# Optimization experiments

Hardware: AMD Instinct MI355X
Metric: run time of the kernel (lower is better)

The kernel has to match this reference:

```python
import jax, jax.numpy as jnp
import numpy as np

B, S, HIDDEN, NH = 2, 2048, 1024, 16
D = HIDDEN // NH  # 64
PHYS_W, CONS_W = 0.2, 0.15
LN_EPS = 1e-5


def _layernorm(x, gamma, beta):
    mu = jnp.mean(x, axis=-1, keepdims=True)
    var = jnp.mean(jnp.square(x - mu), axis=-1, keepdims=True)
    return (x - mu) * jax.lax.rsqrt(var + LN_EPS) * gamma + beta


def setup_inputs() -> dict:
    key = jax.random.key(0)
    ks = jax.random.split(key, 12)
    s = 0.02
    return {
        "cnn_features": jax.random.normal(ks[0], (B, S, HIDDEN), jnp.float32),
        "llm_features": jax.random.normal(ks[1], (B, S, HIDDEN), jnp.float32),
        # Linear weights stored [in, out] so y = x @ W + b (torch's W.T)
        "Wq": jax.random.normal(ks[2], (HIDDEN, HIDDEN), jnp.float32) * s,
        "bq": jnp.zeros((HIDDEN,), jnp.float32),
        "Wk": jax.random.normal(ks[3], (HIDDEN, HIDDEN), jnp.float32) * s,
        "bk": jnp.zeros((HIDDEN,), jnp.float32),
        "Wv": jax.random.normal(ks[4], (HIDDEN, HIDDEN), jnp.float32) * s,
        "bv": jnp.zeros((HIDDEN,), jnp.float32),
        "Wo": jax.random.normal(ks[5], (HIDDEN, HIDDEN), jnp.float32) * s,
        "bo": jnp.zeros((HIDDEN,), jnp.float32),
        "energy_emb": jax.random.normal(ks[6], (1, 1, HIDDEN), jnp.float32),
        "mass_emb": jax.random.normal(ks[7], (1, 1, HIDDEN), jnp.float32),
        "momentum_emb": jax.random.normal(ks[8], (1, 1, HIDDEN), jnp.float32),
        "gamma": jnp.ones((HIDDEN,), jnp.float32),
        "beta": jnp.zeros((HIDDEN,), jnp.float32),
    }


def reference(cnn_features, llm_features, Wq, bq, Wk, bk, Wv, bv, Wo, bo,
              energy_emb, mass_emb, momentum_emb, gamma, beta):
    Bsz, Sc, _ = cnn_features.shape
    Sl = llm_features.shape[1]

    def attn(q_in, kv_in):
        Sq, Sk = q_in.shape[1], kv_in.shape[1]
        Q = (q_in @ Wq + bq).reshape(Bsz, Sq, NH, D).transpose(0, 2, 1, 3)   # bhqd
        K = (kv_in @ Wk + bk).reshape(Bsz, Sk, NH, D).transpose(0, 2, 1, 3)  # bhkd
        V = (kv_in @ Wv + bv).reshape(Bsz, Sk, NH, D).transpose(0, 2, 1, 3)  # bhkd
        scores = jnp.einsum('bhqd,bhkd->bhqk', Q, K) / np.float32(np.sqrt(D))
        # physics biases: require Sq == Sk (elementwise Q*K), shape [B,H,Sq,1]
        energy_bias = jnp.sum(Q * K, axis=-1, keepdims=True) * PHYS_W
        mass_bias = jnp.mean(Q + K, axis=-1, keepdims=True) * CONS_W
        attn_w = jax.nn.softmax(scores + energy_bias + mass_bias, axis=-1)
        attended = jnp.einsum('bhqk,bhkd->bhqd', attn_w, V)
        attended = attended.transpose(0, 2, 1, 3).reshape(Bsz, Sq, HIDDEN)
        out = attended @ Wo + bo
        return _layernorm(q_in + out, gamma, beta)

    phys = jnp.concatenate([
        jnp.broadcast_to(energy_emb, (Bsz, 1, HIDDEN)),
        jnp.broadcast_to(mass_emb, (Bsz, 1, HIDDEN)),
        jnp.broadcast_to(momentum_emb, (Bsz, 1, HIDDEN)),
    ], axis=1)  # [B, 3, HIDDEN]
    aug_cnn = jnp.concatenate([cnn_features, phys], axis=1)  # [B, Sc+3, H]
    aug_llm = jnp.concatenate([llm_features, phys], axis=1)  # [B, Sl+3, H]

    cnn_att = attn(aug_cnn, aug_llm)
    llm_att = attn(aug_llm, aug_cnn)
    return cnn_att[:, :Sc, :], llm_att[:, :Sl, :]
```

## Files before the change

### kernel.cpp

```cpp
#include <hip/hip_runtime.h>

#define BN 2
#define SS 2048
#define SA 2051
#define HID 1024
#define NHD 16
#define DH 64
#define VTLD 8320
#define KSTR 72
#define VSTR 40
#define MFMA16 __builtin_amdgcn_mfma_f32_16x16x32_bf16
#define QSCALE 0.18033688011112042f

typedef __attribute__((ext_vector_type(4))) float floatx4;
typedef __attribute__((ext_vector_type(8))) short bf16x8;
typedef __attribute__((ext_vector_type(2))) unsigned uintx2;

__device__ __forceinline__ float bf2f(short s) {
  union { unsigned u; float f; } v; v.u = ((unsigned)(unsigned short)s) << 16; return v.f;
}
__device__ __forceinline__ short f2bf(float f) {
  union { float f; unsigned u; } v; v.f = f;
  unsigned u = v.u;
  u += 0x7FFF + ((u >> 16) & 1);
  return (short)(u >> 16);
}
__device__ __forceinline__ unsigned pack2(float lo, float hi) {
  unsigned ul = __float_as_uint(lo) + 0x8000u;
  unsigned uh = __float_as_uint(hi) + 0x8000u;
  return __builtin_amdgcn_perm(uh, ul, 0x07060302u);
}
__device__ __forceinline__ unsigned cvtpk(float lo, float hi) {
  unsigned r;
  asm("v_cvt_pk_bf16_f32 %0, %1, %2" : "=v"(r) : "v"(lo), "v"(hi));
  return r;
}
__device__ __forceinline__ float exp2fast(float x) {
#if __has_builtin(__builtin_amdgcn_exp2f)
  return __builtin_amdgcn_exp2f(x);
#else
  float r; asm("v_exp_f32 %0, %1" : "=v"(r) : "v"(x)); return r;
#endif
}
__device__ __forceinline__ uintx2 qtrans(unsigned A, unsigned B) {
  auto t = __builtin_amdgcn_permlane32_swap(A, B, false, false);
  auto u = __builtin_amdgcn_permlane16_swap(t[0], t[1], false, false);
  uintx2 r; r[0] = u[0]; r[1] = u[1];
  return r;
}
__device__ __forceinline__ void gload16(const short* g, short* l) {
  __builtin_amdgcn_global_load_lds(
      (const __attribute__((address_space(1))) void*)g,
      (__attribute__((address_space(3))) void*)l, 16, 0, 0);
}
__device__ __forceinline__ bool in_is_f32(const unsigned* graw) {
  return graw[0] == 0x3F800000u;
}

__global__ __launch_bounds__(256) void convert_in2(
    const void* __restrict__ s0, const void* __restrict__ s1,
    short* __restrict__ dst, const unsigned* __restrict__ graw) {
  if (!in_is_f32(graw)) return;
  const int NF = 4096 * HID;
  int i = (blockIdx.x * 256 + threadIdx.x) * 4;
  const void* s = i < NF ? s0 : s1;
  int j = i < NF ? i : i - NF;
  float4 v = *(const float4*)((const float*)s + j);
  short4 o; o.x = f2bf(v.x); o.y = f2bf(v.y); o.z = f2bf(v.z); o.w = f2bf(v.w);
  *(short4*)(dst + i) = o;
}

__global__ __launch_bounds__(256) void convert_small(
    const void* s0, const void* s1, const void* s2, const void* s3,
    const void* s4, const void* s5, const void* s6, const void* s7,
    const void* s8, short* __restrict__ dst, const unsigned* __restrict__ graw) {
  bool f32 = in_is_f32(graw);
  const void* srcs[9] = {s0, s1, s2, s3, s4, s5, s6, s7, s8};
  const void* s = srcs[blockIdx.x];
  short* d = dst + (size_t)blockIdx.x * 1024;
  for (int i = threadIdx.x; i < 1024; i += 256)
    d[i] = f32 ? f2bf(((const float*)s)[i]) : ((const short*)s)[i];
}

__global__ __launch_bounds__(256) void conv_wt4(
    const void* __restrict__ W0, const void* __restrict__ W1,
    const void* __restrict__ W2, const void* __restrict__ W3,
    short* __restrict__ WT, const unsigned* __restrict__ graw) {
  __shared__ short tile[32][33];
  bool f32 = in_is_f32(graw);
  const void* Ws[4] = {W0, W1, W2, W3};
  const void* W = Ws[blockIdx.z];
  short* dst = WT + (size_t)blockIdx.z * HID * HID;
  int n0 = blockIdx.x * 32, k0 = blockIdx.y * 32;
  int tx = threadIdx.x & 31, ty = threadIdx.x >> 5;
#pragma unroll
  for (int i = 0; i < 4; i++) {
    int k = k0 + ty + i*8;
    short v = f32 ? f2bf(((const float*)W)[(size_t)k * HID + n0 + tx])
                  : ((const short*)W)[(size_t)k * HID + n0 + tx];
    tile[ty + i*8][tx] = v;
  }
  __syncthreads();
#pragma unroll
  for (int i = 0; i < 4; i++)
    dst[(size_t)(n0 + ty + i*8) * HID + k0 + tx] = tile[tx][ty + i*8];
}

__device__ __forceinline__ void gemm_core_3buf(
    const short* apr0, const short* apr1,
    const short* bpr0, const short* bpr1,
    short* sA, short* sB, int wave, int l16, int quad, int msub, int nsub,
    floatx4 acc[4][4]) {
  gload16(apr0, sA + wave*512);              gload16(apr1, sA + 2048 + wave*512);
  gload16(bpr0, sB + wave*512);              gload16(bpr1, sB + 2048 + wave*512);
  gload16(apr0 + 32, sA + 4096 + wave*512);  gload16(apr1 + 32, sA + 4096 + 2048 + wave*512);
  gload16(bpr0 + 32, sB + 4096 + wave*512);  gload16(bpr1 + 32, sB + 4096 + 2048 + wave*512);
  int p8 = ((quad + (l16 >> 1)) & 3) * 8;
  int cur = 0;
  for (int k0 = 0; k0 < HID; k0 += 32) {
    if (k0 + 32 < HID) {
      asm volatile("s_waitcnt vmcnt(4)" ::: "memory");
    } else {
      asm volatile("s_waitcnt vmcnt(0)" ::: "memory");
    }
    __builtin_amdgcn_s_barrier();
    __builtin_amdgcn_sched_barrier(0);
    if (k0 + 64 < HID) {
      int nx = cur == 0 ? 2 : cur - 1;
      gload16(apr0 + k0 + 64, sA + nx*4096 + wave*512);
      gload16(apr1 + k0 + 64, sA + nx*4096 + 2048 + wave*512);
      gload16(bpr0 + k0 + 64, sB + nx*4096 + wave*512);
      gload16(bpr1 + k0 + 64, sB + nx*4096 + 2048 + wave*512);
    }
    const short* cA = sA + cur*4096;
    const short* cB = sB + cur*4096;
    bf16x8 af[4], bf_[4];
#pragma unroll
    for (int i = 0; i < 4; i++) {
      af[i]  = *(const bf16x8*)(cA + (msub + i*16 + l16)*32 + p8);
      bf_[i] = *(const bf16x8*)(cB + (nsub + i*16 + l16)*32 + p8);
    }
#pragma unroll
    for (int mi = 0; mi < 4; mi++)
#pragma unroll
      for (int ni = 0; ni < 4; ni++)
        acc[mi][ni] = MFMA16(af[mi], bf_[ni], acc[mi][ni], 0, 0, 0);
    __builtin_amdgcn_sched_barrier(0);
    cur = cur == 2 ? 0 : cur + 1;
  }
}

__global__ __launch_bounds__(256) void gemm_qkv(
    const short* __restrict__ Xa, const short* __restrict__ WqT,
    const short* __restrict__ WkT, const short* __restrict__ WvT,
    const short* __restrict__ embB, const short* __restrict__ bqB,
    const short* __restrict__ bkB, const short* __restrict__ bvB,
    short* __restrict__ Qa, short* __restrict__ Ka, short* __restrict__ VT,
    const void* __restrict__ cnn, const void* __restrict__ llm,
    const unsigned* __restrict__ graw) {
  __shared__ __align__(16) short sA[3*4096];
  __shared__ __align__(16) short sB[3*4096];
  int t = threadIdx.x;
  int wave = t >> 6, lane = t & 63, l16 = lane & 15, quad = lane >> 4;
  int bid = blockIdx.x;
  int swz = (bid & 7) * 194 + (bid >> 3);
  bool f32 = in_is_f32(graw);

  const short *A, *B, *bias; short* out; long ldc;
  int m0, n0, xA, xB, tailA, tailB, bias_row; float scale;
  if (swz < 512) {
    A = nullptr; B = WqT; bias = bqB; out = Qa; ldc = HID;
    m0 = (swz >> 3) * 128; n0 = (swz & 7) * 128;
    xA = 1; xB = 0; tailA = 0; tailB = 0; bias_row = 0; scale = QSCALE;
  } else if (swz < 1032) {
    int id = swz - 512;
    A = nullptr; B = WkT; bias = bkB; out = Ka; ldc = HID;
    m0 = (id >> 3) * 128; n0 = (id & 7) * 128;
    xA = 1; xB = 0; tailA = 1; tailB = 0; bias_row = 0; scale = 1.f;
  } else {
    int id = swz - 1032;
    A = WvT; B = nullptr; bias = bvB; out = VT; ldc = VTLD;
    m0 = (id / 65) * 128; n0 = (id % 65) * 128;
    xA = 0; xB = 1; tailA = 0; tailB = 1; bias_row = 1; scale = 1.f;
  }
  int msub = (wave >> 1) * 64, nsub = (wave & 1) * 64;

  auto xrow = [&](int r) -> const short* {
    if (f32) return Xa + (size_t)r * HID;
    return r < 4096 ? (const short*)cnn + (size_t)r * HID
                    : (const short*)llm + (size_t)(r - 4096) * HID;
  };
  int kc = (((lane & 3) - ((lane >> 3) & 3)) & 3) * 8;
  const short* apr[2]; const short* bpr[2];
#pragma unroll
  for (int rep = 0; rep < 2; rep++) {
    int cid = rep * 256 + t;
    int row = cid >> 2;
    int ra = m0 + row;
    const short* ap;
    if (xA) ap = (tailA && ra >= 8192)
                   ? embB + (size_t)((ra > 8194 ? 8194 : ra) - 8192) * 1024
                   : xrow(ra);
    else    ap = A + (size_t)ra * HID;
    int rb = n0 + row;
    const short* bp;
    if (xB) bp = (tailB && rb >= 8192)
                   ? embB + (size_t)((rb > 8194 ? 8194 : rb) - 8192) * 1024
                   : xrow(rb);
    else    bp = B + (size_t)rb * HID;
    apr[rep] = ap + kc; bpr[rep] = bp + kc;
  }

  floatx4 acc[4][4] = {};
  gemm_core_3buf(apr[0], apr[1], bpr[0], bpr[1], sA, sB,
                 wave, l16, quad, msub, nsub, acc);

#pragma unroll
  for (int mi = 0; mi < 4; mi++)
#pragma unroll
    for (int ni = 0; ni < 4; ni++) {
      int col = n0 + nsub + ni*16 + l16;
      float bcol = bias_row ? 0.f : bf2f(bias[col]);
#pragma unroll
      for (int r = 0; r < 4; r++) {
        int m = m0 + msub + mi*16 + quad*4 + r;
        float v = (acc[mi][ni][r] + (bias_row ? bf2f(bias[m]) : bcol)) * scale;
        out[(size_t)m * ldc + col] = f2bf(v);
      }
    }
}

__global__ __launch_bounds__(256) void gemm_bf(
    const short* __restrict__ A, const short* __restrict__ B,
    const short* __restrict__ bias, float scale,
    float* __restrict__ out32,
    const void* __restrict__ rc0, const void* __restrict__ rc1,
    const unsigned* __restrict__ graw) {
  __shared__ __align__(16) short sA[3*4096];
  __shared__ __align__(16) short sB[3*4096];
  int t = threadIdx.x;
  int wave = t >> 6, lane = t & 63, l16 = lane & 15, quad = lane >> 4;
  int nwg = gridDim.x * gridDim.y;
  int bid = blockIdx.y * gridDim.x + blockIdx.x;
  int cpx = nwg >> 3;
  int swz = (bid & 7) * cpx + (bid >> 3);
  int bx = swz % gridDim.x, by = swz / gridDim.x;
  int m0 = by * 128, n0 = bx * 128;
  int msub = (wave >> 1) * 64, nsub = (wave & 1) * 64;

  int kc = (((lane & 3) - ((lane >> 3) & 3)) & 3) * 8;
  const short* apr[2]; const short* bpr[2];
#pragma unroll
  for (int rep = 0; rep < 2; rep++) {
    int cid = rep * 256 + t;
    int row = cid >> 2;
    apr[rep] = A + (size_t)(m0 + row) * HID + kc;
    bpr[rep] = B + (size_t)(n0 + row) * HID + kc;
  }

  floatx4 acc[4][4] = {};
  gemm_core_3buf(apr[0], apr[1], bpr[0], bpr[1], sA, sB,
                 wave, l16, quad, msub, nsub, acc);

  bool f32in = in_is_f32(graw);
#pragma unroll
  for (int mi = 0; mi < 4; mi++)
#pragma unroll
    for (int ni = 0; ni < 4; ni++) {
      int col = n0 + nsub + ni*16 + l16;
      float bcol = bf2f(bias[col]);
#pragma unroll
      for (int r = 0; r < 4; r++) {
        int m = m0 + msub + mi*16 + quad*4 + r;
        float v = (acc[mi][ni][r] + bcol) * scale;
        float res;
        if (f32in) res = ((const float*)(m < 4096 ? rc0 : rc1))[(size_t)(m & 4095) * HID + col];
        else       res = bf2f(((const short*)(m < 4096 ? rc0 : rc1))[(size_t)(m & 4095) * HID + col]);
        out32[(size_t)m * HID + col] = v + res;
      }
    }
}

__global__ __launch_bounds__(256, 2) void flash3(
    const short* __restrict__ Qa, const short* __restrict__ Ka,
    const short* __restrict__ VTa, short* __restrict__ att) {
  __shared__ __align__(16) short sK[2][2][32*KSTR];
  __shared__ __align__(16) short sV[2][2][64*VSTR];
  int t = threadIdx.x, wave = t >> 6, lane = t & 63;
  int l16 = lane & 15, quad = lane >> 4;
  int bid = blockIdx.x;
  int swz = (bid & 7) * 64 + (bid >> 3);
  int qt  = swz & 7;
  int h   = (swz >> 3) & 15;
  int sb  = swz >> 7;
  int side = sb >> 1, b = sb & 1;
  int qrow0 = side * 4096 + b * 2048;
  int kvb = (side ^ 1) * 4096 + b * 2048;
  int q0 = qt * 256 + wave * 64;

  bf16x8 qa[4], qb[4];
#pragma unroll
  for (int g = 0; g < 4; g++) {
    const short* qp = Qa + (size_t)(qrow0 + q0 + g*16 + l16) * HID + h*DH + quad*8;
    qa[g] = *(const bf16x8*)qp;
    qb[g] = *(const bf16x8*)(qp + 32);
  }

  float rs[4] = {0.f, 0.f, 0.f, 0.f};
  floatx4 o[4][4] = {};

  int krow = t >> 3, kc8 = (t & 7) * 8;
  int vrow = t >> 2, vc8 = (t & 3) * 8;
  const short* kgp = Ka + (size_t)(kvb + krow) * HID + h*DH + kc8;
  const short* vgp = VTa + (size_t)(h*DH + vrow) * VTLD + kvb + vc8;
  bf16x8 krA = *(const bf16x8*)kgp, krB = *(const bf16x8*)(kgp + 32*HID);
  bf16x8 vrA = *(const bf16x8*)vgp, vrB = *(const bf16x8*)(vgp + 32);
  int ph = 0;

  for (int kv0 = 0; kv0 < 2048; kv0 += 64) {
    *(bf16x8*)(&sK[ph][0][krow*KSTR + kc8]) = krA;
    *(bf16x8*)(&sK[ph][1][krow*KSTR + kc8]) = krB;
    *(bf16x8*)(&sV[ph][0][vrow*VSTR + vc8]) = vrA;
    *(bf16x8*)(&sV[ph][1][vrow*VSTR + vc8]) = vrB;
    __syncthreads();
    kgp += 64*HID; vgp += 64;
    krA = *(const bf16x8*)kgp; krB = *(const bf16x8*)(kgp + 32*HID);
    vrA = *(const bf16x8*)vgp; vrB = *(const bf16x8*)(vgp + 32);

#pragma unroll
    for (int s = 0; s < 2; s++) {
      const short* kw = sK[ph][s];
      const short* vw = sV[ph][s];
      bf16x8 k00 = *(const bf16x8*)(kw + l16*KSTR + quad*8);
      bf16x8 k01 = *(const bf16x8*)(kw + l16*KSTR + 32 + quad*8);
      bf16x8 k10 = *(const bf16x8*)(kw + (16 + l16)*KSTR + quad*8);
      bf16x8 k11 = *(const bf16x8*)(kw + (16 + l16)*KSTR + 32 + quad*8);
      bf16x8 v0 = *(const bf16x8*)(vw + l16*VSTR + quad*8);
      bf16x8 v1 = *(const bf16x8*)(vw + (16 + l16)*VSTR + quad*8);
      bf16x8 v2 = *(const bf16x8*)(vw + (32 + l16)*VSTR + quad*8);
      bf16x8 v3 = *(const bf16x8*)(vw + (48 + l16)*VSTR + quad*8);

#pragma unroll
      for (int g = 0; g < 4; g++) {
        floatx4 s0 = {}, s1 = {};
        __builtin_amdgcn_s_setprio(1);
        s0 = MFMA16(k00, qa[g], s0, 0, 0, 0); s0 = MFMA16(k01, qb[g], s0, 0, 0, 0);
        s1 = MFMA16(k10, qa[g], s1, 0, 0, 0); s1 = MFMA16(k11, qb[g], s1, 0, 0, 0);
        __builtin_amdgcn_s_setprio(0);

        floatx4 p0, p1;
#pragma unroll
        for (int r = 0; r < 4; r++) {
          p0[r] = exp2fast(s0[r]); p1[r] = exp2fast(s1[r]);
        }
        rs[g] += ((p0[0]+p0[1])+(p0[2]+p0[3])) + ((p1[0]+p1[1])+(p1[2]+p1[3]));

        unsigned c0 = cvtpk(p0[0], p0[1]), c1 = cvtpk(p0[2], p0[3]);
        unsigned c2 = cvtpk(p1[0], p1[1]), c3 = cvtpk(p1[2], p1[3]);
        uintx2 u0 = qtrans(c0, c2);
        uintx2 u1 = qtrans(c1, c3);
        union { unsigned u[4]; bf16x8 v; } pf;
        pf.u[0] = u0[0]; pf.u[1] = u1[0]; pf.u[2] = u0[1]; pf.u[3] = u1[1];

        __builtin_amdgcn_s_setprio(1);
        o[g][0] = MFMA16(v0, pf.v, o[g][0], 0, 0, 0);
        o[g][1] = MFMA16(v1, pf.v, o[g][1], 0, 0, 0);
        o[g][2] = MFMA16(v2, pf.v, o[g][2], 0, 0, 0);
        o[g][3] = MFMA16(v3, pf.v, o[g][3], 0, 0, 0);
        __builtin_amdgcn_s_setprio(0);
      }
    }
    ph ^= 1;
  }

  {
    int er = l16 < 2 ? l16 : 2;
    const short* kpt = Ka + (size_t)(8192 + er) * HID + h*DH + quad*8;
    bf16x8 tk0 = *(const bf16x8*)kpt;
    bf16x8 tk1 = *(const bf16x8*)(kpt + 32);
    const short* vtp = VTa + (size_t)(h*DH + l16) * VTLD + 8192 + quad*8;
    bf16x8 v0 = *(const bf16x8*)vtp;
    bf16x8 v1 = *(const bf16x8*)(vtp + 16*VTLD);
    bf16x8 v2 = *(const bf16x8*)(vtp + 32*VTLD);
    bf16x8 v3 = *(const bf16x8*)(vtp + 48*VTLD);
#pragma unroll
    for (int g = 0; g < 4; g++) {
      floatx4 s0 = {};
      s0 = MFMA16(tk0, qa[g], s0, 0, 0, 0); s0 = MFMA16(tk1, qb[g], s0, 0, 0, 0);
      floatx4 p0;
#pragma unroll
      for (int r = 0; r < 4; r++) {
        bool val = (quad == 0) && (r < 3);
        p0[r] = val ? exp2fast(s0[r]) : 0.f;
      }
      rs[g] += (p0[0]+p0[1]) + (p0[2]+p0[3]);
      unsigned c0 = cvtpk(p0[0], p0[1]), c1 = cvtpk(p0[2], p0[3]);
      uintx2 u0 = qtrans(c0, 0u);
      uintx2 u1 = qtrans(c1, 0u);
      union { unsigned u[4]; bf16x8 v; } pf;
      pf.u[0] = u0[0]; pf.u[1] = u1[0]; pf.u[2] = u0[1]; pf.u[3] = u1[1];
      o[g][0] = MFMA16(v0, pf.v, o[g][0], 0, 0, 0);
      o[g][1] = MFMA16(v1, pf.v, o[g][1], 0, 0, 0);
      o[g][2] = MFMA16(v2, pf.v, o[g][2], 0, 0, 0);
      o[g][3] = MFMA16(v3, pf.v, o[g][3], 0, 0, 0);
    }
  }

#pragma unroll
  for (int g = 0; g < 4; g++) {
    float r = rs[g];
    r += __shfl_xor(r, 16, 64); r += __shfl_xor(r, 32, 64);
    float inv = 1.f / r;
    unsigned* ob = (unsigned*)(att + (size_t)(qrow0 + q0 + g*16 + l16) * HID + h*DH + quad*4);
#pragma unroll
    for (int n = 0; n < 4; n++) {
      ob[n*8]     = pack2(o[g][n][0]*inv, o[g][n][1]*inv);
      ob[n*8 + 1] = pack2(o[g][n][2]*inv, o[g][n][3]*inv);
    }
  }
}

__global__ __launch_bounds__(256) void ln_kernel(
    const float* __restrict__ y, const short* __restrict__ gamma,
    const short* __restrict__ beta, void* __restrict__ outp, long orow,
    const unsigned* __restrict__ graw) {
  bool f32o = in_is_f32(graw);
  int row = blockIdx.x;
  int t = threadIdx.x;
  const float* yr = y + (size_t)row * HID;
  float4 v = ((const float4*)yr)[t];
  float sum = v.x + v.y + v.z + v.w;
#pragma unroll
  for (int off = 32; off >= 1; off >>= 1) sum += __shfl_xor(sum, off, 64);
  __shared__ float red[8];
  int wave = t >> 6, lane = t & 63;
  if (lane == 0) red[wave] = sum;
  __syncthreads();
  float mu = (red[0] + red[1] + red[2] + red[3]) * (1.f/HID);
  float dx = v.x - mu, dy = v.y - mu, dz = v.z - mu, dw = v.w - mu;
  float sq = dx*dx + dy*dy + dz*dz + dw*dw;
#pragma unroll
  for (int off = 32; off >= 1; off >>= 1) sq += __shfl_xor(sq, off, 64);
  if (lane == 0) red[4 + wave] = sq;
  __syncthreads();
  float var = (red[4] + red[5] + red[6] + red[7]) * (1.f/HID);
  float inv = rsqrtf(var + 1e-5f);
  const short* g = gamma + t*4;
  const short* be = beta + t*4;
  float o0 = dx * inv * bf2f(g[0]) + bf2f(be[0]);
  float o1 = dy * inv * bf2f(g[1]) + bf2f(be[1]);
  float o2 = dz * inv * bf2f(g[2]) + bf2f(be[2]);
  float o3 = dw * inv * bf2f(g[3]) + bf2f(be[3]);
  size_t base = (size_t)(orow + row) * HID + t*4;
  if (f32o) {
    float4 ov = {o0, o1, o2, o3};
    *(float4*)((float*)outp + base) = ov;
  } else {
    short4 ov = {f2bf(o0), f2bf(o1), f2bf(o2), f2bf(o3)};
    *(short4*)((short*)outp + base) = ov;
  }
}

extern "C" void kernel_launch(void* const* d_in, const int* in_sizes, int n_in,
                              void* d_out, int out_size, void* d_ws, size_t ws_size,
                              hipStream_t stream) {
  const void* cnn = d_in[0];
  const void* llm = d_in[1];
  const void* Wq  = d_in[2];
  const void* bq  = d_in[3];
  const void* Wk  = d_in[4];
  const void* bk  = d_in[5];
  const void* Wv  = d_in[6];
  const void* bv  = d_in[7];
  const void* Wo  = d_in[8];
  const void* bo  = d_in[9];
  const void* ee  = d_in[10];
  const void* me  = d_in[11];
  const void* pe  = d_in[12];
  const void* gamma = d_in[13];
  const void* beta  = d_in[14];
  const unsigned* graw = (const unsigned*)gamma;
  (void)in_sizes; (void)n_in; (void)out_size; (void)ws_size;

  char* p = (char*)d_ws;
  auto alloc = [&](size_t bytes) { char* r = p; p += (bytes + 255) & ~(size_t)255; return r; };
  short* WqT = (short*)alloc((size_t)HID*HID*2);
  short* WkT = (short*)alloc((size_t)HID*HID*2);
  short* WvT = (short*)alloc((size_t)HID*HID*2);
  short* WoT = (short*)alloc((size_t)HID*HID*2);
  short* smallB = (short*)alloc(9 * 1024 * 2);
  short* Qa  = (short*)alloc((size_t)8192 * HID * 2);
  short* Ka  = (short*)alloc((size_t)8320 * HID * 2);
  short* VT  = (short*)alloc((size_t)HID * VTLD * 2);
  float* y   = (float*)Qa;
  short* att = (short*)d_out;
  short* Xa  = (short*)d_out + (size_t)8192 * HID;
  short* bqB = smallB;        short* bkB = smallB + 1024;
  short* bvB = smallB + 2048; short* boB = smallB + 3072;
  short* embB = smallB + 4096;
  short* gB  = smallB + 7168; short* bB  = smallB + 8192;

  dim3 tb(256);
  const int NF = 4096 * HID;

  convert_in2<<<dim3(2*NF/1024), tb, 0, stream>>>(cnn, llm, Xa, graw);
  conv_wt4<<<dim3(32, 32, 4), tb, 0, stream>>>(Wq, Wk, Wv, Wo, WqT, graw);
  convert_small<<<dim3(9), tb, 0, stream>>>(bq, bk, bv, bo, ee, me, pe, gamma, beta,
                                            smallB, graw);

  gemm_qkv<<<dim3(1552), tb, 0, stream>>>(Xa, WqT, WkT, WvT, embB,
                                          bqB, bkB, bvB, Qa, Ka, VT,
                                          cnn, llm, graw);

  flash3<<<dim3(512), tb, 0, stream>>>(Qa, Ka, VT, att);

  gemm_bf<<<dim3(8, 64), tb, 0, stream>>>(att, WoT, boB, 1.f, y, cnn, llm, graw);

  ln_kernel<<<dim3(8192), tb, 0, stream>>>(y, gB, bB, d_out, 0, graw);
}
```

Before: 350.9 us.

## Load K/V tiles directly from global into registers, dropping LDS staging

Replaces the LDS double-buffered K/V staging in the flash attention kernel with per-wave direct global loads into MFMA operand registers, prefetched one 32-key step ahead. This removes the block-wide barrier and the LDS write/read round trip each iteration. In exchange, each wave issues its own redundant global loads for the same K/V data, relying on cache hits, and register pressure rises from the prefetch buffers.

```diff
diff --git a/kernel.cpp b/kernel.cpp
--- a/kernel.cpp
+++ b/kernel.cpp
@@ -7,8 +7,6 @@
 #define NHD 16
 #define DH 64
 #define VTLD 8320
-#define KSTR 72
-#define VSTR 40
 #define MFMA16 __builtin_amdgcn_mfma_f32_16x16x32_bf16
 #define QSCALE 0.18033688011112042f
 
@@ -284,8 +282,6 @@
 __global__ __launch_bounds__(256, 2) void flash3(
     const short* __restrict__ Qa, const short* __restrict__ Ka,
     const short* __restrict__ VTa, short* __restrict__ att) {
-  __shared__ __align__(16) short sK[2][2][32*KSTR];
-  __shared__ __align__(16) short sV[2][2][64*VSTR];
   int t = threadIdx.x, wave = t >> 6, lane = t & 63;
   int l16 = lane & 15, quad = lane >> 4;
   int bid = blockIdx.x;
@@ -309,68 +305,62 @@
   float rs[4] = {0.f, 0.f, 0.f, 0.f};
   floatx4 o[4][4] = {};
 
-  int krow = t >> 3, kc8 = (t & 7) * 8;
-  int vrow = t >> 2, vc8 = (t & 3) * 8;
-  const short* kgp = Ka + (size_t)(kvb + krow) * HID + h*DH + kc8;
-  const short* vgp = VTa + (size_t)(h*DH + vrow) * VTLD + kvb + vc8;
-  bf16x8 krA = *(const bf16x8*)kgp, krB = *(const bf16x8*)(kgp + 32*HID);
-  bf16x8 vrA = *(const bf16x8*)vgp, vrB = *(const bf16x8*)(vgp + 32);
-  int ph = 0;
-
-  for (int kv0 = 0; kv0 < 2048; kv0 += 64) {
-    *(bf16x8*)(&sK[ph][0][krow*KSTR + kc8]) = krA;
-    *(bf16x8*)(&sK[ph][1][krow*KSTR + kc8]) = krB;
-    *(bf16x8*)(&sV[ph][0][vrow*VSTR + vc8]) = vrA;
-    *(bf16x8*)(&sV[ph][1][vrow*VSTR + vc8]) = vrB;
-    __syncthreads();
-    kgp += 64*HID; vgp += 64;
-    krA = *(const bf16x8*)kgp; krB = *(const bf16x8*)(kgp + 32*HID);
-    vrA = *(const bf16x8*)vgp; vrB = *(const bf16x8*)(vgp + 32);
-
-#pragma unroll
-    for (int s = 0; s < 2; s++) {
-      const short* kw = sK[ph][s];
-      const short* vw = sV[ph][s];
-      bf16x8 k00 = *(const bf16x8*)(kw + l16*KSTR + quad*8);
-      bf16x8 k01 = *(const bf16x8*)(kw + l16*KSTR + 32 + quad*8);
-      bf16x8 k10 = *(const bf16x8*)(kw + (16 + l16)*KSTR + quad*8);
-      bf16x8 k11 = *(const bf16x8*)(kw + (16 + l16)*KSTR + 32 + quad*8);
-      bf16x8 v0 = *(const bf16x8*)(vw + l16*VSTR + quad*8);
-      bf16x8 v1 = *(const bf16x8*)(vw + (16 + l16)*VSTR + quad*8);
-      bf16x8 v2 = *(const bf16x8*)(vw + (32 + l16)*VSTR + quad*8);
-      bf16x8 v3 = *(const bf16x8*)(vw + (48 + l16)*VSTR + quad*8);
-
-#pragma unroll
-      for (int g = 0; g < 4; g++) {
-        floatx4 s0 = {}, s1 = {};
-        __builtin_amdgcn_s_setprio(1);
-        s0 = MFMA16(k00, qa[g], s0, 0, 0, 0); s0 = MFMA16(k01, qb[g], s0, 0, 0, 0);
-        s1 = MFMA16(k10, qa[g], s1, 0, 0, 0); s1 = MFMA16(k11, qb[g], s1, 0, 0, 0);
-        __builtin_amdgcn_s_setprio(0);
-
-        floatx4 p0, p1;
-#pragma unroll
-        for (int r = 0; r < 4; r++) {
-          p0[r] = exp2fast(s0[r]); p1[r] = exp2fast(s1[r]);
-        }
-        rs[g] += ((p0[0]+p0[1])+(p0[2]+p0[3])) + ((p1[0]+p1[1])+(p1[2]+p1[3]));
-
-        unsigned c0 = cvtpk(p0[0], p0[1]), c1 = cvtpk(p0[2], p0[3]);
-        unsigned c2 = cvtpk(p1[0], p1[1]), c3 = cvtpk(p1[2], p1[3]);
-        uintx2 u0 = qtrans(c0, c2);
-        uintx2 u1 = qtrans(c1, c3);
-        union { unsigned u[4]; bf16x8 v; } pf;
-        pf.u[0] = u0[0]; pf.u[1] = u1[0]; pf.u[2] = u0[1]; pf.u[3] = u1[1];
-
-        __builtin_amdgcn_s_setprio(1);
-        o[g][0] = MFMA16(v0, pf.v, o[g][0], 0, 0, 0);
-        o[g][1] = MFMA16(v1, pf.v, o[g][1], 0, 0, 0);
-        o[g][2] = MFMA16(v2, pf.v, o[g][2], 0, 0, 0);
-        o[g][3] = MFMA16(v3, pf.v, o[g][3], 0, 0, 0);
-        __builtin_amdgcn_s_setprio(0);
+  const short* kp = Ka + (size_t)(kvb + l16) * HID + h*DH + quad*8;
+  const short* vp = VTa + (size_t)(h*DH + l16) * VTLD + kvb + quad*8;
+  bf16x8 k00 = *(const bf16x8*)kp;
+  bf16x8 k01 = *(const bf16x8*)(kp + 32);
+  bf16x8 k10 = *(const bf16x8*)(kp + 16*HID);
+  bf16x8 k11 = *(const bf16x8*)(kp + 16*HID + 32);
+  bf16x8 v0 = *(const bf16x8*)vp;
+  bf16x8 v1 = *(const bf16x8*)(vp + 16*VTLD);
+  bf16x8 v2 = *(const bf16x8*)(vp + 32*VTLD);
+  bf16x8 v3 = *(const bf16x8*)(vp + 48*VTLD);
+
+  for (int kv0 = 0; kv0 < 2048; kv0 += 32) {
+    const short* kpn = kp + 32*HID;
+    const short* vpn = vp + 32;
+    bf16x8 nk00 = *(const bf16x8*)kpn;
+    bf16x8 nk01 = *(const bf16x8*)(kpn + 32);
+    bf16x8 nk10 = *(const bf16x8*)(kpn + 16*HID);
+    bf16x8 nk11 = *(const bf16x8*)(kpn + 16*HID + 32);
+    bf16x8 nv0 = *(const bf16x8*)vpn;
+    bf16x8 nv1 = *(const bf16x8*)(vpn + 16*VTLD);
+    bf16x8 nv2 = *(const bf16x8*)(vpn + 32*VTLD);
+    bf16x8 nv3 = *(const bf16x8*)(vpn + 48*VTLD);
+
+#pragma unroll
+    for (int g = 0; g < 4; g++) {
+      floatx4 s0 = {}, s1 = {};
+      __builtin_amdgcn_s_setprio(1);
+      s0 = MFMA16(k00, qa[g], s0, 0, 0, 0); s0 = MFMA16(k01, qb[g], s0, 0, 0, 0);
+      s1 = MFMA16(k10, qa[g], s1, 0, 0, 0); s1 = MFMA16(k11, qb[g], s1, 0, 0, 0);
+      __builtin_amdgcn_s_setprio(0);
+
+      floatx4 p0, p1;
+#pragma unroll
+      for (int r = 0; r < 4; r++) {
+        p0[r] = exp2fast(s0[r]); p1[r] = exp2fast(s1[r]);
       }
-    }
-    ph ^= 1;
+      rs[g] += ((p0[0]+p0[1])+(p0[2]+p0[3])) + ((p1[0]+p1[1])+(p1[2]+p1[3]));
+
+      unsigned c0 = cvtpk(p0[0], p0[1]), c1 = cvtpk(p0[2], p0[3]);
+      unsigned c2 = cvtpk(p1[0], p1[1]), c3 = cvtpk(p1[2], p1[3]);
+      uintx2 u0 = qtrans(c0, c2);
+      uintx2 u1 = qtrans(c1, c3);
+      union { unsigned u[4]; bf16x8 v; } pf;
+      pf.u[0] = u0[0]; pf.u[1] = u1[0]; pf.u[2] = u0[1]; pf.u[3] = u1[1];
+
+      __builtin_amdgcn_s_setprio(1);
+      o[g][0] = MFMA16(v0, pf.v, o[g][0], 0, 0, 0);
+      o[g][1] = MFMA16(v1, pf.v, o[g][1], 0, 0, 0);
+      o[g][2] = MFMA16(v2, pf.v, o[g][2], 0, 0, 0);
+      o[g][3] = MFMA16(v3, pf.v, o[g][3], 0, 0, 0);
+      __builtin_amdgcn_s_setprio(0);
+    }
+
+    k00 = nk00; k01 = nk01; k10 = nk10; k11 = nk11;
+    v0 = nv0; v1 = nv1; v2 = nv2; v3 = nv3;
+    kp = kpn; vp = vpn;
   }
 
   {
@@ -379,10 +369,10 @@
     bf16x8 tk0 = *(const bf16x8*)kpt;
     bf16x8 tk1 = *(const bf16x8*)(kpt + 32);
     const short* vtp = VTa + (size_t)(h*DH + l16) * VTLD + 8192 + quad*8;
-    bf16x8 v0 = *(const bf16x8*)vtp;
-    bf16x8 v1 = *(const bf16x8*)(vtp + 16*VTLD);
-    bf16x8 v2 = *(const bf16x8*)(vtp + 32*VTLD);
-    bf16x8 v3 = *(const bf16x8*)(vtp + 48*VTLD);
+    bf16x8 w0 = *(const bf16x8*)vtp;
+    bf16x8 w1 = *(const bf16x8*)(vtp + 16*VTLD);
+    bf16x8 w2 = *(const bf16x8*)(vtp + 32*VTLD);
+    bf16x8 w3 = *(const bf16x8*)(vtp + 48*VTLD);
 #pragma unroll
     for (int g = 0; g < 4; g++) {
       floatx4 s0 = {};
@@ -399,10 +389,10 @@
       uintx2 u1 = qtrans(c1, 0u);
       union { unsigned u[4]; bf16x8 v; } pf;
       pf.u[0] = u0[0]; pf.u[1] = u1[0]; pf.u[2] = u0[1]; pf.u[3] = u1[1];
-      o[g][0] = MFMA16(v0, pf.v, o[g][0], 0, 0, 0);
-      o[g][1] = MFMA16(v1, pf.v, o[g][1], 0, 0, 0);
-      o[g][2] = MFMA16(v2, pf.v, o[g][2], 0, 0, 0);
-      o[g][3] = MFMA16(v3, pf.v, o[g][3], 0, 0, 0);
+      o[g][0] = MFMA16(w0, pf.v, o[g][0], 0, 0, 0);
+      o[g][1] = MFMA16(w1, pf.v, o[g][1], 0, 0, 0);
+      o[g][2] = MFMA16(w2, pf.v, o[g][2], 0, 0, 0);
+      o[g][3] = MFMA16(w3, pf.v, o[g][3], 0, 0, 0);
     }
   }
 
```

Result: slower. 402.6 us (+14.7%).
